# Optimization experiments

Measured on AMD Instinct MI355X. Metric: run time of the kernel, lower is better.

The kernel has to match this reference:

```python
import jax, jax.numpy as jnp
import numpy as np

STRIDE = 8
NUM_POINTS = 17
OFFSET_RANGE = 1.5
NUM_HEADS = 4
BASE_OFFSETS = np.array([(-1,-1),(-1,0),(-1,1),(0,-1),(0,0),(0,1),(1,-1),(1,0),(1,1),
                         (-3,-3),(-3,0),(-3,3),(0,-3),(0,3),(3,-3),(3,0),(3,3)], dtype=np.float32)


def setup_inputs() -> dict:
    key = jax.random.key(0)
    ks = jax.random.split(key, 16)
    N, D, P, B = 40000, 128, NUM_POINTS, 2
    Hf, Wf, H_img, W_img = 56, 100, 448, 800
    x_lidar = jax.random.normal(ks[0], (N, D), jnp.float32)
    b_idx = jax.random.randint(ks[1], (N, 1), 0, B)
    z = jax.random.randint(ks[2], (N, 1), 0, 10)
    y = jax.random.randint(ks[3], (N, 1), 0, 125)
    x = jax.random.randint(ks[4], (N, 1), 0, 125)
    indices = jnp.concatenate([b_idx, z, y, x], axis=1).astype(jnp.int32)
    img_feats = jax.random.normal(ks[5], (B, D, Hf, Wf), jnp.float32)
    voxel_size = jnp.array([0.1, 0.1, 0.1], jnp.float32)
    pc_range = jnp.array([-50.0, -50.0, -5.0, 50.0, 50.0, 3.0], jnp.float32)
    # plausible lidar->image projection: intrinsics @ extrinsics (x-forward -> z-forward)
    K = np.array([[600.0, 0.0, W_img / 2.0], [0.0, 600.0, H_img / 2.0], [0.0, 0.0, 1.0]])
    Rt = np.array([[0.0, -1.0, 0.0, 0.0], [0.0, 0.0, -1.0, 1.5], [1.0, 0.0, 0.0, 0.0]])
    P34 = (K @ Rt).astype(np.float32)
    trans_lidar_to_img = jnp.asarray(np.stack([P34, P34]))
    s = 0.02
    return {
        'x_lidar': x_lidar,
        'indices': indices,
        'img_feats': img_feats,
        'voxel_size': voxel_size,
        'pc_range': pc_range,
        'trans_lidar_to_img': trans_lidar_to_img,
        'offset_W': jax.random.normal(ks[6], (D, 2 * P), jnp.float32) * s,
        'offset_b': jax.random.normal(ks[7], (2 * P,), jnp.float32) * s,
        'q_W': jax.random.normal(ks[8], (D, D), jnp.float32) * s,
        'q_b': jnp.zeros((D,), jnp.float32),
        'k_W': jax.random.normal(ks[9], (D, D), jnp.float32) * s,
        'k_b': jnp.zeros((D,), jnp.float32),
        'v_W': jax.random.normal(ks[10], (D, D), jnp.float32) * s,
        'v_b': jnp.zeros((D,), jnp.float32),
        'out_W': jax.random.normal(ks[11], (D, D), jnp.float32) * s,
        'out_b': jnp.zeros((D,), jnp.float32),
        'H_img': H_img,
        'W_img': W_img,
    }


def _forward(x_lidar, indices, img_feats, voxel_size, pc_range, trans_lidar_to_img,
             offset_W, offset_b, q_W, q_b, k_W, k_b, v_W, v_b, out_W, out_b, H_img, W_img):
    N, D = x_lidar.shape
    B, C, Hf, Wf = img_feats.shape
    bidx = indices[:, 0].astype(jnp.int32)
    # --- project voxel centers to normalized image coords ---
    spatial = indices[:, jnp.array([3, 2, 1])].astype(jnp.float32)  # (x, y, z) order
    cvs = voxel_size * STRIDE
    phys = spatial * cvs + pc_range[:3] + cvs * 0.5                 # [N,3]
    hom = jnp.concatenate([phys, jnp.ones((N, 1), phys.dtype)], axis=1)
    pts = jnp.einsum('nij,nj->ni', trans_lidar_to_img[bidx], hom)   # [N,3]
    depth = jnp.maximum(pts[:, 2], 1e-5)
    u_feat = (pts[:, 0] / depth) * (float(Wf) / float(W_img))
    v_feat = (pts[:, 1] / depth) * (float(Hf) / float(H_img))
    u_n = 2.0 * (u_feat / max(Wf - 1, 1)) - 1.0
    v_n = 2.0 * (v_feat / max(Hf - 1, 1)) - 1.0
    centers = jnp.stack([u_n, v_n], axis=-1)                        # [N,2]
    # --- sampling grid: base ring + learned tanh offsets ---
    du = 2.0 / max(Wf - 1, 1)
    dv = 2.0 / max(Hf - 1, 1)
    base = jnp.asarray(BASE_OFFSETS) * jnp.array([du, dv], jnp.float32)  # [P,2]
    learned = jnp.tanh(x_lidar @ offset_W + offset_b).reshape(N, NUM_POINTS, 2)
    learned = learned * jnp.array([OFFSET_RANGE * du, OFFSET_RANGE * dv], jnp.float32)
    grid = centers[:, None, :] + base[None] + learned               # [N,P,2]
    gx, gy = grid[..., 0], grid[..., 1]
    valid = (jnp.abs(gx) <= 1.0) & (jnp.abs(gy) <= 1.0)             # [N,P]
    # --- bilinear grid_sample, align_corners=True, zeros padding, batched gather ---
    px = (gx + 1.0) * 0.5 * (Wf - 1)
    py = (gy + 1.0) * 0.5 * (Hf - 1)
    x0 = jnp.floor(px).astype(jnp.int32)
    y0 = jnp.floor(py).astype(jnp.int32)
    fx = px - x0
    fy = py - y0
    sampled = jnp.zeros((N, NUM_POINTS, C), x_lidar.dtype)
    for dx_, wx in ((0, 1.0 - fx), (1, fx)):
        for dy_, wy in ((0, 1.0 - fy), (1, fy)):
            xc = x0 + dx_
            yc = y0 + dy_
            inb = (xc >= 0) & (xc < Wf) & (yc >= 0) & (yc < Hf)
            w = wx * wy * inb
            val = img_feats[bidx[:, None], :, jnp.clip(yc, 0, Hf - 1), jnp.clip(xc, 0, Wf - 1)]  # [N,P,C]
            sampled = sampled + val * w[..., None]
    # --- single-query cross attention over sampled points ---
    scale = float(D // NUM_HEADS) ** -0.5
    q = x_lidar @ q_W + q_b                                         # [N,D]
    k = sampled @ k_W + k_b                                         # [N,P,D]
    v = sampled @ v_W + v_b
    attn = jnp.einsum('nd,npd->np', q, k) * scale
    attn = jnp.where(valid, attn, -10000.0)
    attn = jax.nn.softmax(attn, axis=-1)
    attn = attn * valid
    attn = attn / jnp.maximum(attn.sum(-1, keepdims=True), 1e-6)
    out = jnp.einsum('np,npd->nd', attn, v)
    out = out @ out_W + out_b
    # --- rectifier stats ---
    offset_scale = OFFSET_RANGE * max((du ** 2 + dv ** 2) ** 0.5, 1e-6)
    instability = jnp.linalg.norm(learned, axis=-1).mean(-1, keepdims=True) / offset_scale
    offset_stability = jnp.clip(jnp.exp(-instability), 0.0, 1.0)
    valid_sample_ratio = valid.astype(jnp.float32).mean(-1, keepdims=True)
    p = jnp.clip(attn, 1e-6, None)
    entropy = -(p * jnp.log(p)).sum(-1, keepdims=True)
    attn_focus = jnp.clip(1.0 - entropy / float(np.log(max(NUM_POINTS, 2))), 0.0, 1.0)
    return out, valid_sample_ratio, offset_stability, attn_focus


def reference(x_lidar, indices, img_feats, voxel_size, pc_range, trans_lidar_to_img,
              offset_W, offset_b, q_W, q_b, k_W, k_b, v_W, v_b, out_W, out_b, H_img, W_img):
    return _forward(x_lidar, indices, img_feats, voxel_size, pc_range, trans_lidar_to_img,
                    offset_W, offset_b, q_W, q_b, k_W, k_b, v_W, v_b, out_W, out_b, H_img, W_img)
```

## Files before the change

kernel.cpp:

```cpp
#include <hip/hip_runtime.h>
#include <hip/hip_fp16.h>
#include <math.h>

#define NPTS 17
#define DCH 128
#define HF 56
#define WF 100

using half8 = __attribute__((ext_vector_type(8))) _Float16;
using f32x4 = __attribute__((ext_vector_type(4))) float;

#define OFF_WKB    0
#define OFF_A0     128
#define OFF_B0     256
#define OFF_C0     384
#define OFF_W2T    512
#define OFF_BMT    8704
#define OFF_WOFS   16896
#define OFF_FEAT   23040
#define OFF_UVB    739840
#define OFF_IDX    899840
#define OFF_CNT    939840

__device__ inline __half2 bc_h2(unsigned u) { return __builtin_bit_cast(__half2, u); }
__device__ inline unsigned bc_u32(__half2 h) { return __builtin_bit_cast(unsigned, h); }
__device__ inline unsigned packh2(float a, float b) {
  return bc_u32(__float22half2_rn(make_float2(a, b)));
}
__device__ inline ushort f2hu(float x) {
  __half h = __float2half(x);
  return __builtin_bit_cast(ushort, h);
}

__device__ inline int swz(int row, int bcol) {
  return (row << 8) + (bcol ^ ((row & 7) << 4));
}
__device__ inline int swz7(int row, int bcol) {
  return (row << 7) + (bcol ^ ((row & 7) << 4));
}

__device__ inline void project(int4 iv, const float* voxel_size,
    const float* pc_range, const float* trans, float winv, float hinv,
    float& u_n, float& v_n, int& bidx)
{
  bidx = iv.x;
  float cv0 = voxel_size[0]*8.f, cv1 = voxel_size[1]*8.f, cv2 = voxel_size[2]*8.f;
  float ph0 = (float)iv.w*cv0 + pc_range[0] + 0.5f*cv0;
  float ph1 = (float)iv.z*cv1 + pc_range[1] + 0.5f*cv1;
  float ph2 = (float)iv.y*cv2 + pc_range[2] + 0.5f*cv2;
  const float* T = trans + bidx*12;
  float p0 = T[0]*ph0 + T[1]*ph1 + T[2]*ph2  + T[3];
  float p1 = T[4]*ph0 + T[5]*ph1 + T[6]*ph2  + T[7];
  float p2 = T[8]*ph0 + T[9]*ph1 + T[10]*ph2 + T[11];
  float depth = fmaxf(p2, 1e-5f);
  u_n = 2.f*((p0/depth)*winv/99.f) - 1.f;
  v_n = 2.f*((p1/depth)*hinv/55.f) - 1.f;
}

__global__ __launch_bounds__(256) void prep_kernel(
    const float* __restrict__ img,
    const float* __restrict__ q_W, const float* __restrict__ k_W,
    const float* __restrict__ v_W, const float* __restrict__ out_W,
    const float* __restrict__ q_b, const float* __restrict__ k_b,
    const float* __restrict__ v_b,
    const float* __restrict__ offset_W,
    const int* __restrict__ indices,
    const float* __restrict__ voxel_size, const float* __restrict__ pc_range,
    const float* __restrict__ trans,
    const int* __restrict__ HimgP, const int* __restrict__ WimgP,
    float* __restrict__ ws, int N, int nbc)
{
  __shared__ __align__(16) char smraw[32768];
  int tid = threadIdx.x;
  int bid = blockIdx.x;

  if (bid < 224) {
    float* sm = (float*)smraw;
    int by = bid >> 1, ch = bid & 1;
    int b = by / HF, y = by % HF;
    const float* src = img + (size_t)b*DCH*HF*WF + (size_t)ch*64*HF*WF + y*WF;
    #pragma unroll
    for (int i = 0; i < 25; ++i) {
      int flat = i*256 + tid;
      int c = flat / WF;
      int x = flat - c*WF;
      sm[c*101 + x] = src[(size_t)c*HF*WF + x];
    }
    __syncthreads();
    unsigned* dst = (unsigned*)((ushort*)(ws + OFF_FEAT) + (size_t)(b*HF*WF + y*WF)*DCH);
    #pragma unroll
    for (int i = 0; i < 13; ++i) {
      int flat = i*256 + tid;
      if (flat < 3200) {
        int x = flat >> 5;
        int cp = flat & 31;
        dst[(size_t)x*64 + ch*32 + cp] = packh2(sm[(2*cp)*101 + x], sm[(2*cp+1)*101 + x]);
      }
    }
    return;
  }
  bid -= 224;

  if (bid < nbc) {
    int* lc = (int*)smraw;
    int n = bid * 256 + tid;
    bool in = (n < N);
    bool cskip = true;
    if (in) {
      const float du = 2.0f/99.0f, dv = 2.0f/55.0f;
      float winv = (float)WF / (float)(WimgP[0]);
      float hinv = (float)HF / (float)(HimgP[0]);
      float u_n, v_n; int bx;
      project(((const int4*)indices)[n], voxel_size, pc_range, trans, winv, hinv,
              u_n, v_n, bx);
      ((float4*)(ws + OFF_UVB))[n] = make_float4(u_n, v_n, (float)bx, 0.f);
      cskip = (fabsf(u_n) > 1.001f + 4.5f*du) || (fabsf(v_n) > 1.001f + 4.5f*dv);
    }
    if (tid < 2) lc[tid] = 0;
    __syncthreads();
    int my = 0;
    if (in) my = atomicAdd(&lc[cskip ? 1 : 0], 1);
    __syncthreads();
    if (tid < 2) lc[2 + tid] = atomicAdd(&((int*)(ws + OFF_CNT))[tid], lc[tid]);
    __syncthreads();
    if (in) {
      int* idx = (int*)(ws + OFF_IDX);
      if (!cskip) idx[lc[2] + my] = n;
      else        idx[N - 1 - (lc[3] + my)] = n;
    }
    return;
  }
  bid -= nbc;

  if (bid == 0) {
    char* Als = smraw;
    char* Bls = smraw + 16384;
    ushort* w2t = (ushort*)(ws + OFF_W2T);
    int wid = tid >> 6, l = tid & 63, lr = l & 15, lg = l >> 4;
    f32x4 acc[2][8] = {};
    for (int ko = 0; ko < 2; ++ko) {
      __syncthreads();
      #pragma unroll
      for (int i = 0; i < 16; ++i) {
        int flat = i*256 + tid;
        int r = flat >> 5, kp = flat & 31;
        float2 va = *(const float2*)&k_W[r*DCH + ko*64 + 2*kp];
        float2 vb = *(const float2*)&q_W[r*DCH + ko*64 + 2*kp];
        *(unsigned*)(Als + swz7(r, kp*4)) = packh2(va.x, va.y);
        *(unsigned*)(Bls + swz7(r, kp*4)) = packh2(vb.x, vb.y);
      }
      __syncthreads();
      #pragma unroll
      for (int kc = 0; kc < 2; ++kc) {
        int kb = kc*64 + lg*16;
        half8 a0 = *(const half8*)(Als + swz7(wid*32 + lr, kb));
        half8 a1 = *(const half8*)(Als + swz7(wid*32 + 16 + lr, kb));
        #pragma unroll
        for (int ni = 0; ni < 8; ++ni) {
          half8 b = *(const half8*)(Bls + swz7(ni*16 + lr, kb));
          acc[0][ni] = __builtin_amdgcn_mfma_f32_16x16x32_f16(a0, b, acc[0][ni], 0, 0, 0);
          acc[1][ni] = __builtin_amdgcn_mfma_f32_16x16x32_f16(a1, b, acc[1][ni], 0, 0, 0);
        }
      }
    }
    #pragma unroll
    for (int mi = 0; mi < 2; ++mi)
      #pragma unroll
      for (int reg = 0; reg < 4; ++reg) {
        int n = wid*32 + mi*16 + lg*4 + reg;
        #pragma unroll
        for (int ni = 0; ni < 8; ++ni)
          w2t[n*DCH + ni*16 + lr] = f2hu(acc[mi][ni][reg]);
      }
    return;
  }
  bid -= 1;

  if (bid == 0) {
    char* Als = smraw;
    char* Bls = smraw + 16384;
    ushort* bmt = (ushort*)(ws + OFF_BMT);
    int wid = tid >> 6, l = tid & 63, lr = l & 15, lg = l >> 4;
    f32x4 acc[2][8] = {};
    for (int ko = 0; ko < 2; ++ko) {
      __syncthreads();
      #pragma unroll
      for (int i = 0; i < 32; ++i) {
        int flat = i*256 + tid;
        int e = flat >> 7, d = flat & 127;
        float v = out_W[(size_t)(ko*64 + e)*DCH + d];
        *(ushort*)(Als + swz7(d, e*2)) = f2hu(v);
      }
      #pragma unroll
      for (int i = 0; i < 16; ++i) {
        int flat = i*256 + tid;
        int r = flat >> 5, kp = flat & 31;
        float2 vb = *(const float2*)&v_W[r*DCH + ko*64 + 2*kp];
        *(unsigned*)(Bls + swz7(r, kp*4)) = packh2(vb.x, vb.y);
      }
      __syncthreads();
      #pragma unroll
      for (int kc = 0; kc < 2; ++kc) {
        int kb = kc*64 + lg*16;
        half8 a0 = *(const half8*)(Als + swz7(wid*32 + lr, kb));
        half8 a1 = *(const half8*)(Als + swz7(wid*32 + 16 + lr, kb));
        #pragma unroll
        for (int ni = 0; ni < 8; ++ni) {
          half8 b = *(const half8*)(Bls + swz7(ni*16 + lr, kb));
          acc[0][ni] = __builtin_amdgcn_mfma_f32_16x16x32_f16(a0, b, acc[0][ni], 0, 0, 0);
          acc[1][ni] = __builtin_amdgcn_mfma_f32_16x16x32_f16(a1, b, acc[1][ni], 0, 0, 0);
        }
      }
    }
    #pragma unroll
    for (int mi = 0; mi < 2; ++mi)
      #pragma unroll
      for (int reg = 0; reg < 4; ++reg) {
        int d = wid*32 + mi*16 + lg*4 + reg;
        #pragma unroll
        for (int ni = 0; ni < 8; ++ni)
          bmt[d*DCH + ni*16 + lr] = f2hu(acc[mi][ni][reg]);
      }
    return;
  }
  bid -= 1;

  {
    float* vbs = (float*)smraw;
    if (tid < 128) { vbs[tid] = q_b[tid]; vbs[256 + tid] = v_b[tid]; }
    else vbs[tid] = k_b[tid & 127];
    __syncthreads();
    int r = tid & 127;
    const float* M  = (tid < 128) ? k_W : q_W;
    const float* vv = (tid < 128) ? vbs : vbs + 128;
    float acc = 0.f;
    #pragma unroll 8
    for (int e = 0; e < DCH; e += 4) {
      float4 m = *(const float4*)&M[(size_t)r*DCH + e];
      acc += m.x*vv[e] + m.y*vv[e+1] + m.z*vv[e+2] + m.w*vv[e+3];
    }
    ws[((tid < 128) ? OFF_A0 : OFF_WKB) + r] = acc;
    if (tid < 128) {
      float b0 = 0.f;
      #pragma unroll 8
      for (int e = 0; e < DCH; ++e) b0 += vbs[256 + e] * out_W[(size_t)e*DCH + tid];
      ws[OFF_B0 + tid] = b0;
    }
    if (tid < 64) {
      float c = vbs[tid]*vbs[128+tid] + vbs[64+tid]*vbs[192+tid];
      c += __shfl_xor(c, 32); c += __shfl_xor(c, 16); c += __shfl_xor(c, 8);
      c += __shfl_xor(c, 4);  c += __shfl_xor(c, 2);  c += __shfl_xor(c, 1);
      if (tid == 0) ws[OFF_C0] = c;
    }
    ushort* woh = (ushort*)(ws + OFF_WOFS);
    ushort* wol = woh + 48*128;
    #pragma unroll
    for (int i = 0; i < 24; ++i) {
      int flat = i*256 + tid;
      int c = flat >> 7, k = flat & 127;
      float wv = (c < 34) ? offset_W[(size_t)k*34 + c] : 0.f;
      __half hw = __float2half(wv);
      woh[flat] = __builtin_bit_cast(ushort, hw);
      wol[flat] = f2hu(wv - __half2float(hw));
    }
  }
}

__device__ inline void fill_point(float* out, const float* out_b,
                                  float instab, int pt, int mm, int N)
{
  const float du = 2.0f/99.0f, dv = 2.0f/55.0f;
  *(float4*)&out[(size_t)pt*DCH + 8*mm]     = *(const float4*)&out_b[8*mm];
  *(float4*)&out[(size_t)pt*DCH + 8*mm + 4] = *(const float4*)&out_b[8*mm + 4];
  if (mm == 0) {
    out[(size_t)N*128 + pt] = 0.f;
    float osc = 1.5f * sqrtf(du*du + dv*dv);
    float inst = (instab / 17.f) / fmaxf(osc, 1e-6f);
    out[(size_t)N*129 + pt] = fminf(fmaxf(__expf(-inst), 0.f), 1.f);
    float ent = 17.f * 1.3815511e-5f;
    out[(size_t)N*130 + pt] = fminf(fmaxf(1.f - ent / logf(17.f), 0.f), 1.f);
  }
}

__global__ __launch_bounds__(256) void fuse_kernel(
    const float* __restrict__ X,
    const float* __restrict__ offset_b,
    const float* __restrict__ out_b,
    float* __restrict__ ws, float* __restrict__ out, int N)
{
  __shared__ __align__(16) char B_lds[32768];
  __shared__ __align__(16) char A_lds[4096];
  __shared__ __align__(16) char Q_lds[4096];
  __shared__ float lrn_lds[16][36];
  __shared__ float sa_lds[16];

  int tid  = threadIdx.x;
  int wave = tid >> 6, lane = tid & 63;
  int g = lane >> 4, mm = lane & 15;
  int lr = lane & 15, lg = lane >> 4;
  int n0 = blockIdx.x * 16;
  int nvalid = ((const int*)(ws + OFF_CNT))[0];
  const int* idxp = (const int*)(ws + OFF_IDX);
  int slot = n0 + wave*4 + g;
  int row  = wave*4 + g;

  {
    int r  = tid >> 4;
    int k0 = (tid & 15) * 8;
    int sl = n0 + r; if (sl >= N) sl = N - 1;
    int pr = idxp[sl];
    const float* xp = &X[(size_t)pr*DCH + k0];
    float4 v0 = *(const float4*)xp;
    float4 v1 = *(const float4*)(xp + 4);
    __half h0 = __float2half(v0.x), h1 = __float2half(v0.y);
    __half h2 = __float2half(v0.z), h3 = __float2half(v0.w);
    __half h4 = __float2half(v1.x), h5 = __float2half(v1.y);
    __half h6 = __float2half(v1.z), h7 = __float2half(v1.w);
    uint4 hw;
    hw.x = bc_u32(__halves2half2(h0, h1)); hw.y = bc_u32(__halves2half2(h2, h3));
    hw.z = bc_u32(__halves2half2(h4, h5)); hw.w = bc_u32(__halves2half2(h6, h7));
    uint4 lw;
    lw.x = packh2(v0.x - __half2float(h0), v0.y - __half2float(h1));
    lw.y = packh2(v0.z - __half2float(h2), v0.w - __half2float(h3));
    lw.z = packh2(v1.x - __half2float(h4), v1.y - __half2float(h5));
    lw.w = packh2(v1.z - __half2float(h6), v1.w - __half2float(h7));
    *(uint4*)(A_lds + swz(r, k0*2)) = hw;
    *(uint4*)(Q_lds + swz(r, k0*2)) = lw;
  }
  {
    const ushort* woh = (const ushort*)(ws + OFF_WOFS);
    const ushort* wol = woh + 48*128;
    #pragma unroll
    for (int i = 0; i < 3; ++i) {
      int flat = i*256 + tid;
      int r = flat >> 4, kq = (flat & 15) * 8;
      *(uint4*)(B_lds + swz(r, kq*2))         = *(const uint4*)&woh[r*128 + kq];
      *(uint4*)(B_lds + 12288 + swz(r, kq*2)) = *(const uint4*)&wol[r*128 + kq];
    }
  }
  __syncthreads();

  const float du = 2.0f/99.0f, dv = 2.0f/55.0f;

  if (wave < 3) {
    f32x4 acc = {};
    #pragma unroll
    for (int kc = 0; kc < 4; ++kc) {
      int kb = kc*64 + lg*16;
      half8 ah = *(const half8*)(A_lds + swz(lr, kb));
      half8 al = *(const half8*)(Q_lds + swz(lr, kb));
      half8 bh = *(const half8*)(B_lds + swz(wave*16 + lr, kb));
      half8 bl = *(const half8*)(B_lds + 12288 + swz(wave*16 + lr, kb));
      acc = __builtin_amdgcn_mfma_f32_16x16x32_f16(al, bh, acc, 0, 0, 0);
      acc = __builtin_amdgcn_mfma_f32_16x16x32_f16(ah, bl, acc, 0, 0, 0);
      acc = __builtin_amdgcn_mfma_f32_16x16x32_f16(ah, bh, acc, 0, 0, 0);
    }
    int o = wave*16 + lr;
    if (o < 34) {
      float sc = (o & 1) ? 1.5f*dv : 1.5f*du;
      float ob = offset_b[o];
      #pragma unroll
      for (int reg = 0; reg < 4; ++reg)
        lrn_lds[lg*4 + reg][o] = tanhf(acc[reg] + ob) * sc;
    }
  }

  float ck;
  {
    uint4 xr = *(const uint4*)(A_lds + swz(row, 16*mm));
    const float* wk = ws + OFF_WKB + 8*mm;
    __half2 x01 = bc_h2(xr.x), x23 = bc_h2(xr.y), x45 = bc_h2(xr.z), x67 = bc_h2(xr.w);
    float s = __low2float(x01)*wk[0] + __high2float(x01)*wk[1]
            + __low2float(x23)*wk[2] + __high2float(x23)*wk[3]
            + __low2float(x45)*wk[4] + __high2float(x45)*wk[5]
            + __low2float(x67)*wk[6] + __high2float(x67)*wk[7];
    s += __shfl_xor(s, 8); s += __shfl_xor(s, 4);
    s += __shfl_xor(s, 2); s += __shfl_xor(s, 1);
    ck = s + ws[OFF_C0];
  }
  __syncthreads();

  float instab;
  {
    float a = lrn_lds[row][2*mm], b = lrn_lds[row][2*mm + 1];
    float s = sqrtf(a*a + b*b);
    if (mm == 0) {
      float a2 = lrn_lds[row][32], b2 = lrn_lds[row][33];
      s += sqrtf(a2*a2 + b2*b2);
    }
    s += __shfl_xor(s, 1); s += __shfl_xor(s, 2);
    s += __shfl_xor(s, 4); s += __shfl_xor(s, 8);
    instab = s;
  }

  if (n0 >= nvalid) {
    if (slot < N) fill_point(out, out_b, instab, idxp[slot], mm, N);
    return;
  }

  {
    const ushort* w2t = (const ushort*)(ws + OFF_W2T);
    #pragma unroll
    for (int i = 0; i < 8; ++i) {
      int flat = i*2048 + tid*8;
      int r = flat >> 7, k = flat & 127;
      *(uint4*)(B_lds + swz(r, k*2)) = *(const uint4*)&w2t[(size_t)r*DCH + k];
    }
  }
  __syncthreads();

  {
    f32x4 qacc[2] = {};
    #pragma unroll
    for (int kc = 0; kc < 4; ++kc) {
      int kb = kc*64 + lg*16;
      half8 a  = *(const half8*)(A_lds + swz(lr, kb));
      half8 b0 = *(const half8*)(B_lds + swz(wave*32 + lr, kb));
      half8 b1 = *(const half8*)(B_lds + swz(wave*32 + 16 + lr, kb));
      qacc[0] = __builtin_amdgcn_mfma_f32_16x16x32_f16(a, b0, qacc[0], 0, 0, 0);
      qacc[1] = __builtin_amdgcn_mfma_f32_16x16x32_f16(a, b1, qacc[1], 0, 0, 0);
    }
    #pragma unroll
    for (int ni = 0; ni < 2; ++ni)
      #pragma unroll
      for (int reg = 0; reg < 4; ++reg) {
        int r = lg*4 + reg;
        int c = wave*32 + ni*16 + lr;
        *(ushort*)(Q_lds + swz(r, c*2)) = f2hu(qacc[ni][reg] + ws[OFF_A0 + c]);
      }
  }
  __syncthreads();

  {
    const ushort* bmt = (const ushort*)(ws + OFF_BMT);
    #pragma unroll
    for (int i = 0; i < 8; ++i) {
      int flat = i*2048 + tid*8;
      int r = flat >> 7, k = flat & 127;
      *(uint4*)(B_lds + swz(r, k*2)) = *(const uint4*)&bmt[(size_t)r*DCH + k];
    }
  }

  if (slot >= nvalid) {
    if (mm == 0) sa_lds[row] = 0.f;
    uint4 z; z.x = 0u; z.y = 0u; z.z = 0u; z.w = 0u;
    *(uint4*)(Q_lds + swz(row, 16*mm)) = z;
    if (slot < N) fill_point(out, out_b, instab, idxp[slot], mm, N);
  } else {
    int pt = idxp[slot];
    float4 uv = ((const float4*)(ws + OFF_UVB))[pt];
    float u_n = uv.x, v_n = uv.y;
    int bidx = (int)uv.z;

    uint4 qp = *(const uint4*)(Q_lds + swz(row, 16*mm));
    __half2 q01 = bc_h2(qp.x), q23 = bc_h2(qp.y), q45 = bc_h2(qp.z), q67 = bc_h2(qp.w);

    const float BOX[NPTS] = {-1,-1,-1, 0,0,0, 1,1,1, -3,-3,-3, 0,0, 3,3,3};
    const float BOY[NPTS] = {-1, 0, 1,-1,0,1,-1,0,1, -3, 0, 3, -3,3,-3,0,3};
    const float scale = 0.17677669529663689f;
    const char* fb = (const char*)(ws + OFF_FEAT);

    float larr[NPTS];
    unsigned vm = 0;
    float m_run = -1e28f, srun = 0.f;
    __half2 pre01 = __float2half2_rn(0.f), pre23 = __float2half2_rn(0.f);
    __half2 pre45 = __float2half2_rn(0.f), pre67 = __float2half2_rn(0.f);
    int fbase = bidx * (HF*WF);
    int moff = mm * 16;

    #pragma unroll
    for (int p = 0; p < NPTS; ++p) {
      float2 lrn = *(const float2*)&lrn_lds[row][2*p];
      float gx = u_n + BOX[p]*du + lrn.x;
      float gy = v_n + BOY[p]*dv + lrn.y;
      bool valid = (fabsf(gx) <= 1.f) && (fabsf(gy) <= 1.f);
      float l = -1e30f;
      if (valid) {
        vm |= (1u << p);
        float px = fmaf(gx, 49.5f, 49.5f);
        float py = fmaf(gy, 27.5f, 27.5f);
        float fpx = floorf(px), fpy = floorf(py);
        float fx = px - fpx, fy = py - fpy;
        int x0 = (int)fpx, y0 = (int)fpy;
        int x1 = min(x0 + 1, WF - 1), y1 = min(y0 + 1, HF - 1);
        float wy0 = 1.f - fy, wx0 = 1.f - fx;
        __half2 h00 = __float2half2_rn(wy0*wx0);
        __half2 h01 = __float2half2_rn(wy0*fx);
        __half2 h10 = __float2half2_rn(fy*wx0);
        __half2 h11 = __float2half2_rn(fy*fx);
        int r0 = (fbase + y0*WF) << 8, r1 = (fbase + y1*WF) << 8;
        uint4 f00 = *(const uint4*)(fb + r0 + (x0 << 8) + moff);
        uint4 f01 = *(const uint4*)(fb + r0 + (x1 << 8) + moff);
        uint4 f10 = *(const uint4*)(fb + r1 + (x0 << 8) + moff);
        uint4 f11 = *(const uint4*)(fb + r1 + (x1 << 8) + moff);
        __half2 s01 = __hfma2(h00, bc_h2(f00.x),
                      __hfma2(h01, bc_h2(f01.x),
                      __hfma2(h10, bc_h2(f10.x),
                      __hmul2(h11, bc_h2(f11.x)))));
        __half2 s23 = __hfma2(h00, bc_h2(f00.y),
                      __hfma2(h01, bc_h2(f01.y),
                      __hfma2(h10, bc_h2(f10.y),
                      __hmul2(h11, bc_h2(f11.y)))));
        __half2 s45 = __hfma2(h00, bc_h2(f00.z),
                      __hfma2(h01, bc_h2(f01.z),
                      __hfma2(h10, bc_h2(f10.z),
                      __hmul2(h11, bc_h2(f11.z)))));
        __half2 s67 = __hfma2(h00, bc_h2(f00.w),
                      __hfma2(h01, bc_h2(f01.w),
                      __hfma2(h10, bc_h2(f10.w),
                      __hmul2(h11, bc_h2(f11.w)))));
        __half2 dh = __hfma2(s01, q01, __hfma2(s23, q23,
                     __hfma2(s45, q45, __hmul2(s67, q67))));
        float part = __low2float(dh) + __high2float(dh);
        part += __shfl_xor(part, 8);
        part += __shfl_xor(part, 4);
        part += __shfl_xor(part, 2);
        part += __shfl_xor(part, 1);
        l = (part + ck) * scale;
        float nm  = fmaxf(m_run, l);
        float esc = __expf(m_run - nm);
        float a   = __expf(l - nm);
        m_run = nm;
        srun = srun*esc + a;
        __half2 esch = __float2half2_rn(esc);
        __half2 ah   = __float2half2_rn(a);
        pre01 = __hfma2(ah, s01, __hmul2(pre01, esch));
        pre23 = __hfma2(ah, s23, __hmul2(pre23, esch));
        pre45 = __hfma2(ah, s45, __hmul2(pre45, esch));
        pre67 = __hfma2(ah, s67, __hmul2(pre67, esch));
      }
      larr[p] = l;
    }

    bool anyv = (vm != 0);
    float offv = anyv ? (m_run + __logf(srun)) : 1e38f;
    float invs = anyv ? 1.f/srun : 0.f;
    __half2 ih = __float2half2_rn(invs);
    pre01 = __hmul2(pre01, ih);
    pre23 = __hmul2(pre23, ih);
    pre45 = __hmul2(pre45, ih);
    pre67 = __hmul2(pre67, ih);

    float ent = 0.f;
    #pragma unroll
    for (int p = 0; p < NPTS; ++p) {
      float d = offv - larr[p];
      float a = __expf(-d);
      ent += (a >= 1e-6f) ? a*d : 1.3815511e-5f;
    }

    uint4 pw;
    pw.x = bc_u32(pre01);
    pw.y = bc_u32(pre23);
    pw.z = bc_u32(pre45);
    pw.w = bc_u32(pre67);
    *(uint4*)(Q_lds + swz(row, 16*mm)) = pw;
    if (mm == 0) {
      sa_lds[row] = anyv ? 1.f : 0.f;
      out[(size_t)N*128 + pt] = (float)__popc(vm) / 17.f;
      float osc = 1.5f * sqrtf(du*du + dv*dv);
      float inst = (instab / 17.f) / fmaxf(osc, 1e-6f);
      out[(size_t)N*129 + pt] = fminf(fmaxf(__expf(-inst), 0.f), 1.f);
      out[(size_t)N*130 + pt] = fminf(fmaxf(1.f - ent / logf(17.f), 0.f), 1.f);
    }
  }
  __syncthreads();

  {
    f32x4 oacc[2] = {};
    #pragma unroll
    for (int kc = 0; kc < 4; ++kc) {
      int kb = kc*64 + lg*16;
      half8 a  = *(const half8*)(Q_lds + swz(lr, kb));
      half8 b0 = *(const half8*)(B_lds + swz(wave*32 + lr, kb));
      half8 b1 = *(const half8*)(B_lds + swz(wave*32 + 16 + lr, kb));
      oacc[0] = __builtin_amdgcn_mfma_f32_16x16x32_f16(a, b0, oacc[0], 0, 0, 0);
      oacc[1] = __builtin_amdgcn_mfma_f32_16x16x32_f16(a, b1, oacc[1], 0, 0, 0);
    }
    #pragma unroll
    for (int reg = 0; reg < 4; ++reg) {
      int r = lg*4 + reg;
      int sl2 = n0 + r;
      if (sl2 >= nvalid) continue;
      int p2 = idxp[sl2];
      float sa = sa_lds[r];
      #pragma unroll
      for (int ni = 0; ni < 2; ++ni) {
        int c = wave*32 + ni*16 + lr;
        out[(size_t)p2*DCH + c] = oacc[ni][reg] + sa*ws[OFF_B0 + c] + out_b[c];
      }
    }
  }
}

extern "C" void kernel_launch(void* const* d_in, const int* in_sizes, int n_in,
                              void* d_out, int out_size, void* d_ws, size_t ws_size,
                              hipStream_t stream) {
  const float* x_lidar    = (const float*)d_in[0];
  const int*   indices    = (const int*)  d_in[1];
  const float* img        = (const float*)d_in[2];
  const float* voxel_size = (const float*)d_in[3];
  const float* pc_range   = (const float*)d_in[4];
  const float* trans      = (const float*)d_in[5];
  const float* offset_W   = (const float*)d_in[6];
  const float* offset_b   = (const float*)d_in[7];
  const float* q_W        = (const float*)d_in[8];
  const float* q_b        = (const float*)d_in[9];
  const float* k_W        = (const float*)d_in[10];
  const float* k_b        = (const float*)d_in[11];
  const float* v_W        = (const float*)d_in[12];
  const float* v_b        = (const float*)d_in[13];
  const float* out_W      = (const float*)d_in[14];
  const float* out_b      = (const float*)d_in[15];
  const int*   Himg       = (const int*)  d_in[16];
  const int*   Wimg       = (const int*)  d_in[17];
  float* ws  = (float*)d_ws;
  float* out = (float*)d_out;
  int N = in_sizes[0] / DCH;
  int nbc = (N + 255) / 256;

  hipMemsetAsync(ws + OFF_CNT, 0, 2*sizeof(int), stream);
  hipLaunchKernelGGL(prep_kernel, dim3(224 + nbc + 3), dim3(256), 0, stream,
                     img, q_W, k_W, v_W, out_W, q_b, k_b, v_b,
                     offset_W, indices, voxel_size, pc_range, trans,
                     Himg, Wimg, ws, N, nbc);
  hipLaunchKernelGGL(fuse_kernel, dim3((N + 15) / 16), dim3(256), 0, stream,
                     x_lidar, offset_b, out_b, ws, out, N);
}
```

Before: 45.98 us.

## Read MFMA weight operands directly from global memory instead of staging in LDS

Removes the 32KB shared-memory B buffer and the cooperative copies of the offset, q-projection and output weight matrices into LDS. Each MFMA now loads its B fragments straight from global/L2, which also drops one block barrier. The point's projected uv and index are loaded earlier to overlap with the q GEMM. This cuts LDS usage, which may raise occupancy, and removes the staging work. The cost is redundant global loads of the weights per block that depend on L1/L2 hit rates.

```diff
diff --git a/kernel.cpp b/kernel.cpp
--- a/kernel.cpp
+++ b/kernel.cpp
@@ -288,7 +288,6 @@
     const float* __restrict__ out_b,
     float* __restrict__ ws, float* __restrict__ out, int N)
 {
-  __shared__ __align__(16) char B_lds[32768];
   __shared__ __align__(16) char A_lds[4096];
   __shared__ __align__(16) char Q_lds[4096];
   __shared__ float lrn_lds[16][36];
@@ -327,30 +326,22 @@
     *(uint4*)(A_lds + swz(r, k0*2)) = hw;
     *(uint4*)(Q_lds + swz(r, k0*2)) = lw;
   }
-  {
-    const ushort* woh = (const ushort*)(ws + OFF_WOFS);
-    const ushort* wol = woh + 48*128;
-    #pragma unroll
-    for (int i = 0; i < 3; ++i) {
-      int flat = i*256 + tid;
-      int r = flat >> 4, kq = (flat & 15) * 8;
-      *(uint4*)(B_lds + swz(r, kq*2))         = *(const uint4*)&woh[r*128 + kq];
-      *(uint4*)(B_lds + 12288 + swz(r, kq*2)) = *(const uint4*)&wol[r*128 + kq];
-    }
-  }
   __syncthreads();
 
   const float du = 2.0f/99.0f, dv = 2.0f/55.0f;
+  const ushort* wofs = (const ushort*)(ws + OFF_WOFS);
 
   if (wave < 3) {
     f32x4 acc = {};
     #pragma unroll
     for (int kc = 0; kc < 4; ++kc) {
-      int kb = kc*64 + lg*16;
+      int kb  = kc*64 + lg*16;
+      int kel = kc*32 + lg*8;
       half8 ah = *(const half8*)(A_lds + swz(lr, kb));
       half8 al = *(const half8*)(Q_lds + swz(lr, kb));
-      half8 bh = *(const half8*)(B_lds + swz(wave*16 + lr, kb));
-      half8 bl = *(const half8*)(B_lds + 12288 + swz(wave*16 + lr, kb));
+      const ushort* wb = &wofs[(size_t)(wave*16 + lr)*DCH + kel];
+      half8 bh = *(const half8*)wb;
+      half8 bl = *(const half8*)(wb + 48*DCH);
       acc = __builtin_amdgcn_mfma_f32_16x16x32_f16(al, bh, acc, 0, 0, 0);
       acc = __builtin_amdgcn_mfma_f32_16x16x32_f16(ah, bl, acc, 0, 0, 0);
       acc = __builtin_amdgcn_mfma_f32_16x16x32_f16(ah, bh, acc, 0, 0, 0);
@@ -398,25 +389,23 @@
     return;
   }
 
+  float u_n = 0.f, v_n = 0.f; int bidx = 0; int pt = -1;
+  if (slot < nvalid) {
+    pt = idxp[slot];
+    float4 uv = ((const float4*)(ws + OFF_UVB))[pt];
+    u_n = uv.x; v_n = uv.y; bidx = (int)uv.z;
+  }
+
   {
     const ushort* w2t = (const ushort*)(ws + OFF_W2T);
-    #pragma unroll
-    for (int i = 0; i < 8; ++i) {
-      int flat = i*2048 + tid*8;
-      int r = flat >> 7, k = flat & 127;
-      *(uint4*)(B_lds + swz(r, k*2)) = *(const uint4*)&w2t[(size_t)r*DCH + k];
-    }
-  }
-  __syncthreads();
-
-  {
     f32x4 qacc[2] = {};
     #pragma unroll
     for (int kc = 0; kc < 4; ++kc) {
-      int kb = kc*64 + lg*16;
+      int kb  = kc*64 + lg*16;
+      int kel = kc*32 + lg*8;
       half8 a  = *(const half8*)(A_lds + swz(lr, kb));
-      half8 b0 = *(const half8*)(B_lds + swz(wave*32 + lr, kb));
-      half8 b1 = *(const half8*)(B_lds + swz(wave*32 + 16 + lr, kb));
+      half8 b0 = *(const half8*)&w2t[(size_t)(wave*32 + lr)*DCH + kel];
+      half8 b1 = *(const half8*)&w2t[(size_t)(wave*32 + 16 + lr)*DCH + kel];
       qacc[0] = __builtin_amdgcn_mfma_f32_16x16x32_f16(a, b0, qacc[0], 0, 0, 0);
       qacc[1] = __builtin_amdgcn_mfma_f32_16x16x32_f16(a, b1, qacc[1], 0, 0, 0);
     }
@@ -430,16 +419,6 @@
       }
   }
   __syncthreads();
-
-  {
-    const ushort* bmt = (const ushort*)(ws + OFF_BMT);
-    #pragma unroll
-    for (int i = 0; i < 8; ++i) {
-      int flat = i*2048 + tid*8;
-      int r = flat >> 7, k = flat & 127;
-      *(uint4*)(B_lds + swz(r, k*2)) = *(const uint4*)&bmt[(size_t)r*DCH + k];
-    }
-  }
 
   if (slot >= nvalid) {
     if (mm == 0) sa_lds[row] = 0.f;
@@ -447,11 +426,6 @@
     *(uint4*)(Q_lds + swz(row, 16*mm)) = z;
     if (slot < N) fill_point(out, out_b, instab, idxp[slot], mm, N);
   } else {
-    int pt = idxp[slot];
-    float4 uv = ((const float4*)(ws + OFF_UVB))[pt];
-    float u_n = uv.x, v_n = uv.y;
-    int bidx = (int)uv.z;
-
     uint4 qp = *(const uint4*)(Q_lds + swz(row, 16*mm));
     __half2 q01 = bc_h2(qp.x), q23 = bc_h2(qp.y), q45 = bc_h2(qp.z), q67 = bc_h2(qp.w);
 
@@ -567,13 +541,15 @@
   __syncthreads();
 
   {
+    const ushort* bmt = (const ushort*)(ws + OFF_BMT);
     f32x4 oacc[2] = {};
     #pragma unroll
     for (int kc = 0; kc < 4; ++kc) {
-      int kb = kc*64 + lg*16;
+      int kb  = kc*64 + lg*16;
+      int kel = kc*32 + lg*8;
       half8 a  = *(const half8*)(Q_lds + swz(lr, kb));
-      half8 b0 = *(const half8*)(B_lds + swz(wave*32 + lr, kb));
-      half8 b1 = *(const half8*)(B_lds + swz(wave*32 + 16 + lr, kb));
+      half8 b0 = *(const half8*)&bmt[(size_t)(wave*32 + lr)*DCH + kel];
+      half8 b1 = *(const half8*)&bmt[(size_t)(wave*32 + 16 + lr)*DCH + kel];
       oacc[0] = __builtin_amdgcn_mfma_f32_16x16x32_f16(a, b0, oacc[0], 0, 0, 0);
       oacc[1] = __builtin_amdgcn_mfma_f32_16x16x32_f16(a, b1, oacc[1], 0, 0, 0);
     }
```

After: 49.93 us. 8.6% more time.

## Split image transpose finer and batch point compaction with wave ballots

Applied to the files above, without the earlier changes.

The image-transpose blocks now each handle 32 channels instead of 64, doubling the block count to spread the fp16 layout conversion across more CUs. The point-classification blocks now process 1024 points each, using wave ballots and popcount to replace per-thread shared atomics. A single packed 64-bit global atomic updates both counters at once. UV records are written only for points that are not skipped. The aim is lower atomic contention and better load balance in the prep kernel, at the cost of more registers per thread and fewer compaction blocks.

```diff
diff --git a/kernel.cpp b/kernel.cpp
--- a/kernel.cpp
+++ b/kernel.cpp
@@ -74,59 +74,89 @@
   int tid = threadIdx.x;
   int bid = blockIdx.x;
 
-  if (bid < 224) {
+  if (bid < 448) {
     float* sm = (float*)smraw;
-    int by = bid >> 1, ch = bid & 1;
+    int by = bid >> 2, q = bid & 3;
     int b = by / HF, y = by % HF;
-    const float* src = img + (size_t)b*DCH*HF*WF + (size_t)ch*64*HF*WF + y*WF;
-    #pragma unroll
-    for (int i = 0; i < 25; ++i) {
-      int flat = i*256 + tid;
-      int c = flat / WF;
-      int x = flat - c*WF;
-      sm[c*101 + x] = src[(size_t)c*HF*WF + x];
-    }
-    __syncthreads();
-    unsigned* dst = (unsigned*)((ushort*)(ws + OFF_FEAT) + (size_t)(b*HF*WF + y*WF)*DCH);
+    const float* src = img + (size_t)b*DCH*HF*WF + (size_t)q*32*HF*WF + y*WF;
     #pragma unroll
     for (int i = 0; i < 13; ++i) {
       int flat = i*256 + tid;
       if (flat < 3200) {
-        int x = flat >> 5;
-        int cp = flat & 31;
-        dst[(size_t)x*64 + ch*32 + cp] = packh2(sm[(2*cp)*101 + x], sm[(2*cp+1)*101 + x]);
+        int c = flat / WF;
+        int x = flat - c*WF;
+        sm[c*101 + x] = src[(size_t)c*HF*WF + x];
+      }
+    }
+    __syncthreads();
+    unsigned* dst = (unsigned*)((ushort*)(ws + OFF_FEAT) + (size_t)(b*HF*WF + y*WF)*DCH);
+    #pragma unroll
+    for (int i = 0; i < 7; ++i) {
+      int flat = i*256 + tid;
+      if (flat < 1600) {
+        int x = flat >> 4;
+        int cp = flat & 15;
+        dst[(size_t)x*64 + q*16 + cp] = packh2(sm[(2*cp)*101 + x], sm[(2*cp+1)*101 + x]);
       }
     }
     return;
   }
-  bid -= 224;
+  bid -= 448;
 
   if (bid < nbc) {
     int* lc = (int*)smraw;
-    int n = bid * 256 + tid;
-    bool in = (n < N);
-    bool cskip = true;
-    if (in) {
-      const float du = 2.0f/99.0f, dv = 2.0f/55.0f;
-      float winv = (float)WF / (float)(WimgP[0]);
-      float hinv = (float)HF / (float)(HimgP[0]);
-      float u_n, v_n; int bx;
-      project(((const int4*)indices)[n], voxel_size, pc_range, trans, winv, hinv,
-              u_n, v_n, bx);
-      ((float4*)(ws + OFF_UVB))[n] = make_float4(u_n, v_n, (float)bx, 0.f);
-      cskip = (fabsf(u_n) > 1.001f + 4.5f*du) || (fabsf(v_n) > 1.001f + 4.5f*dv);
-    }
+    int lane = tid & 63;
+    unsigned long long lmlt = (1ull << lane) - 1ull;
+    const float du = 2.0f/99.0f, dv = 2.0f/55.0f;
+    float winv = (float)WF / (float)(WimgP[0]);
+    float hinv = (float)HF / (float)(HimgP[0]);
     if (tid < 2) lc[tid] = 0;
     __syncthreads();
-    int my = 0;
-    if (in) my = atomicAdd(&lc[cskip ? 1 : 0], 1);
+    int myslot[4];
+    bool inA[4], skipA[4];
+    #pragma unroll
+    for (int j = 0; j < 4; ++j) {
+      int n = bid*1024 + j*256 + tid;
+      bool in = (n < N);
+      bool cskip = true;
+      if (in) {
+        float u_n, v_n; int bx;
+        project(((const int4*)indices)[n], voxel_size, pc_range, trans, winv, hinv,
+                u_n, v_n, bx);
+        cskip = (fabsf(u_n) > 1.001f + 4.5f*du) || (fabsf(v_n) > 1.001f + 4.5f*dv);
+        if (!cskip)
+          ((float4*)(ws + OFF_UVB))[n] = make_float4(u_n, v_n, (float)bx, 0.f);
+      }
+      inA[j] = in; skipA[j] = cskip;
+      unsigned long long mv = __ballot(in && !cskip);
+      unsigned long long ms = __ballot(in && cskip);
+      int wv = 0, wsk = 0;
+      if (lane == 0) {
+        wv  = atomicAdd(&lc[0], (int)__popcll(mv));
+        wsk = atomicAdd(&lc[1], (int)__popcll(ms));
+      }
+      wv  = __shfl(wv, 0);
+      wsk = __shfl(wsk, 0);
+      myslot[j] = cskip ? (wsk + (int)__popcll(ms & lmlt))
+                        : (wv  + (int)__popcll(mv & lmlt));
+    }
     __syncthreads();
-    if (tid < 2) lc[2 + tid] = atomicAdd(&((int*)(ws + OFF_CNT))[tid], lc[tid]);
+    if (tid == 0) {
+      unsigned long long pk = (unsigned long long)(unsigned)lc[0]
+                            | ((unsigned long long)(unsigned)lc[1] << 32);
+      unsigned long long old = atomicAdd((unsigned long long*)(ws + OFF_CNT), pk);
+      lc[2] = (int)(unsigned)old;
+      lc[3] = (int)(unsigned)(old >> 32);
+    }
     __syncthreads();
-    if (in) {
-      int* idx = (int*)(ws + OFF_IDX);
-      if (!cskip) idx[lc[2] + my] = n;
-      else        idx[N - 1 - (lc[3] + my)] = n;
+    int* idx = (int*)(ws + OFF_IDX);
+    #pragma unroll
+    for (int j = 0; j < 4; ++j) {
+      int n = bid*1024 + j*256 + tid;
+      if (inA[j]) {
+        if (!skipA[j]) idx[lc[2] + myslot[j]] = n;
+        else           idx[N - 1 - (lc[3] + myslot[j])] = n;
+      }
     }
     return;
   }
@@ -617,10 +647,10 @@
   float* ws  = (float*)d_ws;
   float* out = (float*)d_out;
   int N = in_sizes[0] / DCH;
-  int nbc = (N + 255) / 256;
+  int nbc = (N + 1023) / 1024;
 
   hipMemsetAsync(ws + OFF_CNT, 0, 2*sizeof(int), stream);
-  hipLaunchKernelGGL(prep_kernel, dim3(224 + nbc + 3), dim3(256), 0, stream,
+  hipLaunchKernelGGL(prep_kernel, dim3(448 + nbc + 3), dim3(256), 0, stream,
                      img, q_W, k_W, v_W, out_W, q_b, k_b, v_b,
                      offset_W, indices, voxel_size, pc_range, trans,
                      Himg, Wimg, ws, N, nbc);
```

Result: slower. 47.45 us (+3.2%).
